# Kernel tuning notes

Hardware: AMD Instinct MI355X
Metric: run time of the kernel (lower is better)

## Reference

```python
import jax, jax.numpy as jnp
import numpy as np

B, S, D = 8, 2048, 512
UNITS = 512

def setup_inputs() -> dict:
    key = jax.random.key(0)
    k1, k2, k3, k4 = jax.random.split(key, 4)
    x = jax.random.normal(k1, (B, S, D), dtype=jnp.float32)
    # glorot-like scale for weights
    scale = 1.0 / np.sqrt(D)
    W_q = jax.random.normal(k2, (D, UNITS), dtype=jnp.float32) * scale
    W_k = jax.random.normal(k3, (D, UNITS), dtype=jnp.float32) * scale
    W_v = jax.random.normal(k4, (D, UNITS), dtype=jnp.float32) * scale
    return {"x": x, "W_q": W_q, "W_k": W_k, "W_v": W_v}

def reference(x, W_q, W_k, W_v):
    # Q,K,V: [B,S,U]
    Q = jnp.einsum('bsd,du->bsu', x, W_q)
    Km = jnp.einsum('bsd,du->bsu', x, W_k)
    V = jnp.einsum('bsd,du->bsu', x, W_v)
    units = W_q.shape[-1]
    # scores: [B,S,S] = Q @ K^T / sqrt(units)
    scores = jnp.einsum('bqu,bku->bqk', Q, Km) / jnp.sqrt(jnp.float32(units))
    attn = jax.nn.softmax(scores, axis=-1)
    # output: [B,S,U]
    return jnp.einsum('bqk,bku->bqu', attn, V)
```

## Files before the change

kernel.cpp:

```cpp
#include <hip/hip_runtime.h>
#include <math.h>

#define BN 8
#define SN 2048
#define DN 512
#define UN 512
#define MN (BN*SN)

typedef _Float16 f16;
typedef _Float16 f16x8 __attribute__((ext_vector_type(8)));
typedef _Float16 f16x4 __attribute__((ext_vector_type(4)));
typedef _Float16 f16x2 __attribute__((ext_vector_type(2)));
typedef float    f32x4 __attribute__((ext_vector_type(4)));

#define SCALE 0.044194173824159216f
#define LOG2E 1.4426950408889634f
#define DEFER_THR 8.0f

#define CVT_PK(a, b) __builtin_bit_cast(f16x2, __builtin_amdgcn_cvt_pkrtz((a), (b)))

#define BAR_LGKM() do {                                         \
  asm volatile("s_waitcnt lgkmcnt(0)" ::: "memory");            \
  __builtin_amdgcn_s_barrier();                                 \
  __builtin_amdgcn_sched_barrier(0);                            \
} while (0)

__device__ __forceinline__ void gload_lds16(const f16* g, f16* l) {
  __builtin_amdgcn_global_load_lds(
      (const __attribute__((address_space(1))) unsigned int*)g,
      (__attribute__((address_space(3))) unsigned int*)l, 16, 0, 0);
}

__global__ __launch_bounds__(256) void cvt_w_kernel(const float* __restrict__ Wq,
                                                    const float* __restrict__ Wk,
                                                    const float* __restrict__ Wv,
                                                    f16* __restrict__ Wt) {
  const float* W = blockIdx.y == 0 ? Wq : (blockIdx.y == 1 ? Wk : Wv);
  const float s = blockIdx.y == 0 ? SCALE : 1.0f;
  f16* o = Wt + (size_t)blockIdx.y * DN * UN;
  int t = blockIdx.x * 256 + threadIdx.x;
  int r  = t >> 7;
  int c4 = (t & 127) * 4;
  float4 v = *(const float4*)(W + (size_t)r * UN + c4);
  o[(size_t)(c4 + 0) * DN + r] = (f16)(v.x * s);
  o[(size_t)(c4 + 1) * DN + r] = (f16)(v.y * s);
  o[(size_t)(c4 + 2) * DN + r] = (f16)(v.z * s);
  o[(size_t)(c4 + 3) * DN + r] = (f16)(v.w * s);
}

__global__ __launch_bounds__(256) void qkv_gemm(const float* __restrict__ x,
                                                const f16* __restrict__ Wt,
                                                f16* __restrict__ Qh,
                                                f16* __restrict__ Kh,
                                                f16* __restrict__ Vt) {
  __shared__ __align__(16) f16 As[128 * 32];
  __shared__ __align__(16) f16 Bs[128 * 32];

  const int tid = threadIdx.x;
  const int w = tid >> 6, lane = tid & 63;
  const int l15 = lane & 15, lh = lane >> 4;
  const int m0 = blockIdx.x * 128;
  const int n0 = blockIdx.y * 128;
  const int widx = blockIdx.z;
  const f16* Wbase = Wt + (size_t)widx * DN * UN;

  const int wr = (w >> 1) * 64, wc = (w & 1) * 64;
  f32x4 acc[4][4] = {};

  const int ra = tid >> 1, ha = tid & 1;
  const int akey = (ra >> 1) & 3;
  const int s0 = (ha * 2) ^ akey, s1 = (ha * 2 + 1) ^ akey;
  const float* xrow = x + (size_t)(m0 + ra) * DN + ha * 16;

  for (int kk = 0; kk < 16; ++kk) {
    const int k0 = kk * 32;

#pragma unroll
    for (int q = 0; q < 2; ++q) {
      int j = q * 256 + tid;
      int r = j >> 2, cs = j & 3;
      int c = cs ^ ((r >> 1) & 3);
      f16* bbase = &Bs[(q * 256 + w * 64) * 8];
      gload_lds16(Wbase + (size_t)(n0 + r) * DN + k0 + c * 8, bbase);
    }

    {
      const float* xs = xrow + k0;
      float4 f0 = *(const float4*)(xs + 0);
      float4 f1 = *(const float4*)(xs + 4);
      float4 f2 = *(const float4*)(xs + 8);
      float4 f3 = *(const float4*)(xs + 12);
      f16x8 lo = { (f16)f0.x, (f16)f0.y, (f16)f0.z, (f16)f0.w,
                   (f16)f1.x, (f16)f1.y, (f16)f1.z, (f16)f1.w };
      f16x8 hi = { (f16)f2.x, (f16)f2.y, (f16)f2.z, (f16)f2.w,
                   (f16)f3.x, (f16)f3.y, (f16)f3.z, (f16)f3.w };
      *(f16x8*)&As[ra * 32 + s0 * 8] = lo;
      *(f16x8*)&As[ra * 32 + s1 * 8] = hi;
    }
    __syncthreads();

    f16x8 a[4], bfr[4];
#pragma unroll
    for (int m = 0; m < 4; ++m) {
      int row = wr + m * 16 + l15;
      int ch = lh ^ ((row >> 1) & 3);
      a[m] = *(const f16x8*)&As[row * 32 + ch * 8];
    }
#pragma unroll
    for (int n = 0; n < 4; ++n) {
      int row = wc + n * 16 + l15;
      int ch = lh ^ ((row >> 1) & 3);
      bfr[n] = *(const f16x8*)&Bs[row * 32 + ch * 8];
    }
#pragma unroll
    for (int m = 0; m < 4; ++m)
#pragma unroll
      for (int n = 0; n < 4; ++n)
        acc[m][n] = __builtin_amdgcn_mfma_f32_16x16x32_f16(a[m], bfr[n], acc[m][n], 0, 0, 0);
    __syncthreads();
  }

  if (widx == 2) {
#pragma unroll
    for (int m = 0; m < 4; ++m) {
      int g = m0 + wr + m * 16 + lh * 4;
      int bb = g >> 11;
      int ss = g & 2047;
#pragma unroll
      for (int n = 0; n < 4; ++n) {
        int u = n0 + wc + n * 16 + l15;
        f16x4 pv = { (f16)acc[m][n][0], (f16)acc[m][n][1],
                     (f16)acc[m][n][2], (f16)acc[m][n][3] };
        *(f16x4*)(Vt + ((size_t)bb * UN + u) * SN + ss) = pv;
      }
    }
  } else {
    f16* O = (widx == 0) ? Qh : Kh;
#pragma unroll
    for (int m = 0; m < 4; ++m)
#pragma unroll
      for (int n = 0; n < 4; ++n)
#pragma unroll
        for (int j = 0; j < 4; ++j)
          O[(size_t)(m0 + wr + m * 16 + lh * 4 + j) * UN + (n0 + wc + n * 16 + l15)] =
              (f16)acc[m][n][j];
  }
}

__global__ __launch_bounds__(512, 2) void attn_kernel(const f16* __restrict__ Qh,
                                                      const f16* __restrict__ Kh,
                                                      const f16* __restrict__ Vt,
                                                      float* __restrict__ out) {
  __shared__ __align__(16) f16 Ks[2][64 * 512];
  __shared__ __align__(16) f16 Ps[2][64 * 72];
  __shared__ float redm[2][4][16];
  __shared__ float redl[2][4][16];

  const int tid = threadIdx.x;
  const int w = tid >> 6, lane = tid & 63;
  const int l15 = lane & 15, lh = lane >> 4;
  const int bid = blockIdx.x;
  const int b = bid & 7;
  const int q0 = (bid >> 3) * 64;
  const int rb = w >> 1;
  const int cs = w & 1;

  const f16* Kbat = Kh + (size_t)b * SN * DN;
  const f16* Vbat = Vt + (size_t)b * UN * SN;

  const f16* Qbase = Qh + (size_t)(b * SN + q0 + rb * 16 + l15) * DN;
  f16x8 qf[16];
#pragma unroll
  for (int kc = 0; kc < 16; ++kc)
    qf[kc] = *(const f16x8*)(Qbase + kc * 32 + lh * 8);

  f32x4 acc[4][4] = {};
  float mj[4] = { -1e30f, -1e30f, -1e30f, -1e30f };
  float rsA[4] = { 1.f, 1.f, 1.f, 1.f };
  bool pend = false;
  float mrow = -1e30f, lrow = 0.f;

  const f16* vbase = Vbat + (size_t)(w * 64 + l15) * SN + lh * 8;
  f16x8 vreg[4][2];

#pragma unroll
  for (int q = 0; q < 8; ++q) {
    int r = w * 8 + q;
    gload_lds16(Kbat + (size_t)r * DN + (lane ^ (r & 7)) * 8, &Ks[0][r * 512]);
  }
  asm volatile("s_waitcnt vmcnt(0)" ::: "memory");
  __builtin_amdgcn_s_barrier();
  __builtin_amdgcn_sched_barrier(0);

  const int kswz = l15 & 7;

  for (int t = 0; t < 32; ++t) {
    const int cur = t & 1;
    const int kv0 = t * 64;

    if (t < 31) {
#pragma unroll
      for (int q = 0; q < 8; ++q) {
        int r = w * 8 + q;
        gload_lds16(Kbat + (size_t)(kv0 + 64 + r) * DN + (lane ^ (r & 7)) * 8,
                    &Ks[cur ^ 1][r * 512]);
      }
    }

    f32x4 sc0 = {}, sc1 = {};
    const int r0 = cs * 32 + l15;
    __builtin_amdgcn_s_setprio(1);
#pragma unroll
    for (int kc = 0; kc < 16; ++kc) {
      int ch = ((kc * 4 + lh) ^ kswz) * 8;
      f16x8 k0 = *(const f16x8*)&Ks[cur][r0 * 512 + ch];
      f16x8 k1 = *(const f16x8*)&Ks[cur][(r0 + 16) * 512 + ch];
      sc0 = __builtin_amdgcn_mfma_f32_16x16x32_f16(k0, qf[kc], sc0, 0, 0, 0);
      sc1 = __builtin_amdgcn_mfma_f32_16x16x32_f16(k1, qf[kc], sc1, 0, 0, 0);
    }
    __builtin_amdgcn_s_setprio(0);

    float pm = fmaxf(fmaxf(fmaxf(sc0[0], sc0[1]), fmaxf(sc0[2], sc0[3])),
                     fmaxf(fmaxf(sc1[0], sc1[1]), fmaxf(sc1[2], sc1[3])));
    pm = fmaxf(pm, __shfl_xor(pm, 16, 64));
    pm = fmaxf(pm, __shfl_xor(pm, 32, 64));
    if (lh == 0) redm[cs][rb][l15] = pm;
    BAR_LGKM();

    if (t > 0) {
      if (pend) {
#pragma unroll
        for (int qt = 0; qt < 4; ++qt)
#pragma unroll
          for (int ut = 0; ut < 4; ++ut) {
            acc[ut][qt][0] *= rsA[qt]; acc[ut][qt][1] *= rsA[qt];
            acc[ut][qt][2] *= rsA[qt]; acc[ut][qt][3] *= rsA[qt];
          }
        pend = false;
      }
      __builtin_amdgcn_s_setprio(1);
#pragma unroll
      for (int ks = 0; ks < 2; ++ks) {
#pragma unroll
        for (int qt = 0; qt < 4; ++qt) {
          f16x8 pf = *(const f16x8*)&Ps[cur ^ 1][(qt * 16 + l15) * 72 + ks * 32 + lh * 8];
#pragma unroll
          for (int ut = 0; ut < 4; ++ut)
            acc[ut][qt] = __builtin_amdgcn_mfma_f32_16x16x32_f16(vreg[ut][ks], pf,
                                                                 acc[ut][qt], 0, 0, 0);
        }
      }
      __builtin_amdgcn_s_setprio(0);
    }

#pragma unroll
    for (int ut = 0; ut < 4; ++ut)
#pragma unroll
      for (int ks = 0; ks < 2; ++ks)
        vreg[ut][ks] = *(const f16x8*)(vbase + (size_t)(ut * 16) * SN + kv0 + ks * 32);

    float mn[4];
    bool need = false;
#pragma unroll
    for (int qt = 0; qt < 4; ++qt) {
      mn[qt] = fmaxf(mj[qt], fmaxf(redm[0][qt][l15], redm[1][qt][l15]));
      need = need || (mn[qt] > mj[qt] + DEFER_THR);
    }
    if (__any(need)) {
#pragma unroll
      for (int qt = 0; qt < 4; ++qt) {
        rsA[qt] = exp2f((mj[qt] - mn[qt]) * LOG2E);
        mj[qt] = mn[qt];
      }
      pend = true;
      float rsr = exp2f((mrow - mj[rb]) * LOG2E);
      mrow = mj[rb];
      lrow *= rsr;
    }

    float p[8];
#pragma unroll
    for (int j = 0; j < 4; ++j) {
      p[j]     = exp2f((sc0[j] - mrow) * LOG2E);
      p[4 + j] = exp2f((sc1[j] - mrow) * LOG2E);
    }
    float ts = (p[0] + p[1]) + (p[2] + p[3]) + (p[4] + p[5]) + (p[6] + p[7]);
    ts += __shfl_xor(ts, 16, 64);
    ts += __shfl_xor(ts, 32, 64);
    lrow += ts;

    const int pbase = (rb * 16 + l15) * 72 + cs * 32 + lh * 4;
    *(f16x2*)&Ps[cur][pbase +  0] = CVT_PK(p[0], p[1]);
    *(f16x2*)&Ps[cur][pbase +  2] = CVT_PK(p[2], p[3]);
    *(f16x2*)&Ps[cur][pbase + 16] = CVT_PK(p[4], p[5]);
    *(f16x2*)&Ps[cur][pbase + 18] = CVT_PK(p[6], p[7]);

    asm volatile("s_waitcnt vmcnt(8) lgkmcnt(0)" ::: "memory");
    __builtin_amdgcn_s_barrier();
    __builtin_amdgcn_sched_barrier(0);
  }

  if (pend) {
#pragma unroll
    for (int qt = 0; qt < 4; ++qt)
#pragma unroll
      for (int ut = 0; ut < 4; ++ut) {
        acc[ut][qt][0] *= rsA[qt]; acc[ut][qt][1] *= rsA[qt];
        acc[ut][qt][2] *= rsA[qt]; acc[ut][qt][3] *= rsA[qt];
      }
  }
#pragma unroll
  for (int ks = 0; ks < 2; ++ks) {
#pragma unroll
    for (int qt = 0; qt < 4; ++qt) {
      f16x8 pf = *(const f16x8*)&Ps[1][(qt * 16 + l15) * 72 + ks * 32 + lh * 8];
#pragma unroll
      for (int ut = 0; ut < 4; ++ut)
        acc[ut][qt] = __builtin_amdgcn_mfma_f32_16x16x32_f16(vreg[ut][ks], pf,
                                                             acc[ut][qt], 0, 0, 0);
    }
  }

  if (lh == 0) redl[cs][rb][l15] = lrow;
  __syncthreads();
#pragma unroll
  for (int qt = 0; qt < 4; ++qt) {
    float linv = 1.0f / (redl[0][qt][l15] + redl[1][qt][l15]);
    float* orow = out + (size_t)(b * SN + q0 + qt * 16 + l15) * UN + w * 64 + lh * 4;
#pragma unroll
    for (int ut = 0; ut < 4; ++ut) {
      f32x4 o = acc[ut][qt];
      o[0] *= linv; o[1] *= linv; o[2] *= linv; o[3] *= linv;
      *(f32x4*)(orow + ut * 16) = o;
    }
  }
}

extern "C" void kernel_launch(void* const* d_in, const int* in_sizes, int n_in,
                              void* d_out, int out_size, void* d_ws, size_t ws_size,
                              hipStream_t stream) {
  const float* x  = (const float*)d_in[0];
  const float* Wq = (const float*)d_in[1];
  const float* Wk = (const float*)d_in[2];
  const float* Wv = (const float*)d_in[3];
  float* out = (float*)d_out;

  f16* Wt  = (f16*)d_ws;
  f16* Qh  = Wt + (size_t)3 * DN * UN;
  f16* Kh  = Qh + (size_t)MN * UN;
  f16* Vt  = Kh + (size_t)MN * UN;

  cvt_w_kernel<<<dim3(256, 3), 256, 0, stream>>>(Wq, Wk, Wv, Wt);
  qkv_gemm<<<dim3(128, 4, 3), 256, 0, stream>>>(x, Wt, Qh, Kh, Vt);
  attn_kernel<<<256, 512, 0, stream>>>(Qh, Kh, Vt, out);
}
```

Before: 195.4 us.

## Warp-specialize attention into QK/softmax and PV/load wave groups

The attention block is split into 16 waves: 8 waves compute QK^T scores and softmax, and 8 waves issue the K prefetch, load V and run the PV MFMAs. The two groups sync through LDS barriers, so score computation for one tile overlaps the PV accumulation of the previous tile. Register pressure per wave drops because each wave holds only Q fragments or only V/accumulators. The cost is 1024-thread blocks, more barrier traffic, and a possible loss of occupancy if the launch bound of 4 blocks cannot be met given the LDS size.

After: 528.3 us. +170.4%, slower.

```diff
diff --git a/kernel.cpp b/kernel.cpp
--- a/kernel.cpp
+++ b/kernel.cpp
@@ -18,12 +18,6 @@
 #define DEFER_THR 8.0f
 
 #define CVT_PK(a, b) __builtin_bit_cast(f16x2, __builtin_amdgcn_cvt_pkrtz((a), (b)))
-
-#define BAR_LGKM() do {                                         \
-  asm volatile("s_waitcnt lgkmcnt(0)" ::: "memory");            \
-  __builtin_amdgcn_s_barrier();                                 \
-  __builtin_amdgcn_sched_barrier(0);                            \
-} while (0)
 
 __device__ __forceinline__ void gload_lds16(const f16* g, f16* l) {
   __builtin_amdgcn_global_load_lds(
@@ -74,7 +68,6 @@
 
   for (int kk = 0; kk < 16; ++kk) {
     const int k0 = kk * 32;
-
 #pragma unroll
     for (int q = 0; q < 2; ++q) {
       int j = q * 256 + tid;
@@ -83,7 +76,6 @@
       f16* bbase = &Bs[(q * 256 + w * 64) * 8];
       gload_lds16(Wbase + (size_t)(n0 + r) * DN + k0 + c * 8, bbase);
     }
-
     {
       const float* xs = xrow + k0;
       float4 f0 = *(const float4*)(xs + 0);
@@ -147,10 +139,10 @@
   }
 }
 
-__global__ __launch_bounds__(512, 2) void attn_kernel(const f16* __restrict__ Qh,
-                                                      const f16* __restrict__ Kh,
-                                                      const f16* __restrict__ Vt,
-                                                      float* __restrict__ out) {
+__global__ __launch_bounds__(1024, 4) void attn_kernel(const f16* __restrict__ Qh,
+                                                       const f16* __restrict__ Kh,
+                                                       const f16* __restrict__ Vt,
+                                                       float* __restrict__ out) {
   __shared__ __align__(16) f16 Ks[2][64 * 512];
   __shared__ __align__(16) f16 Ps[2][64 * 72];
   __shared__ float redm[2][4][16];
@@ -162,102 +154,117 @@
   const int bid = blockIdx.x;
   const int b = bid & 7;
   const int q0 = (bid >> 3) * 64;
-  const int rb = w >> 1;
+  const bool qk = (w < 8);
+  const int rb = (w >> 1) & 3;
   const int cs = w & 1;
+  const int wp = w & 7;
 
   const f16* Kbat = Kh + (size_t)b * SN * DN;
   const f16* Vbat = Vt + (size_t)b * UN * SN;
 
-  const f16* Qbase = Qh + (size_t)(b * SN + q0 + rb * 16 + l15) * DN;
+#pragma unroll
+  for (int q = 0; q < 4; ++q) {
+    int r = w * 4 + q;
+    gload_lds16(Kbat + (size_t)r * DN + (lane ^ (r & 7)) * 8, &Ks[0][r * 512]);
+  }
+
   f16x8 qf[16];
-#pragma unroll
-  for (int kc = 0; kc < 16; ++kc)
-    qf[kc] = *(const f16x8*)(Qbase + kc * 32 + lh * 8);
-
+  f16x8 vreg[4][2];
   f32x4 acc[4][4] = {};
   float mj[4] = { -1e30f, -1e30f, -1e30f, -1e30f };
   float rsA[4] = { 1.f, 1.f, 1.f, 1.f };
   bool pend = false;
   float mrow = -1e30f, lrow = 0.f;
 
-  const f16* vbase = Vbat + (size_t)(w * 64 + l15) * SN + lh * 8;
-  f16x8 vreg[4][2];
-
-#pragma unroll
-  for (int q = 0; q < 8; ++q) {
-    int r = w * 8 + q;
-    gload_lds16(Kbat + (size_t)r * DN + (lane ^ (r & 7)) * 8, &Ks[0][r * 512]);
-  }
-  asm volatile("s_waitcnt vmcnt(0)" ::: "memory");
+  const f16* vbase = Vbat + (size_t)(wp * 64 + l15) * SN + lh * 8;
+
+  if (qk) {
+    const f16* Qbase = Qh + (size_t)(b * SN + q0 + rb * 16 + l15) * DN;
+#pragma unroll
+    for (int kc = 0; kc < 16; ++kc)
+      qf[kc] = *(const f16x8*)(Qbase + kc * 32 + lh * 8);
+    asm volatile("s_waitcnt vmcnt(16)" ::: "memory");
+  } else {
+#pragma unroll
+    for (int ut = 0; ut < 4; ++ut)
+#pragma unroll
+      for (int ks = 0; ks < 2; ++ks)
+        vreg[ut][ks] = *(const f16x8*)(vbase + (size_t)(ut * 16) * SN + ks * 32);
+    asm volatile("s_waitcnt vmcnt(8)" ::: "memory");
+  }
   __builtin_amdgcn_s_barrier();
   __builtin_amdgcn_sched_barrier(0);
 
   const int kswz = l15 & 7;
+  f32x4 sc0, sc1;
 
   for (int t = 0; t < 32; ++t) {
     const int cur = t & 1;
     const int kv0 = t * 64;
 
-    if (t < 31) {
-#pragma unroll
-      for (int q = 0; q < 8; ++q) {
-        int r = w * 8 + q;
-        gload_lds16(Kbat + (size_t)(kv0 + 64 + r) * DN + (lane ^ (r & 7)) * 8,
-                    &Ks[cur ^ 1][r * 512]);
-      }
-    }
-
-    f32x4 sc0 = {}, sc1 = {};
-    const int r0 = cs * 32 + l15;
-    __builtin_amdgcn_s_setprio(1);
-#pragma unroll
-    for (int kc = 0; kc < 16; ++kc) {
-      int ch = ((kc * 4 + lh) ^ kswz) * 8;
-      f16x8 k0 = *(const f16x8*)&Ks[cur][r0 * 512 + ch];
-      f16x8 k1 = *(const f16x8*)&Ks[cur][(r0 + 16) * 512 + ch];
-      sc0 = __builtin_amdgcn_mfma_f32_16x16x32_f16(k0, qf[kc], sc0, 0, 0, 0);
-      sc1 = __builtin_amdgcn_mfma_f32_16x16x32_f16(k1, qf[kc], sc1, 0, 0, 0);
-    }
-    __builtin_amdgcn_s_setprio(0);
-
-    float pm = fmaxf(fmaxf(fmaxf(sc0[0], sc0[1]), fmaxf(sc0[2], sc0[3])),
-                     fmaxf(fmaxf(sc1[0], sc1[1]), fmaxf(sc1[2], sc1[3])));
-    pm = fmaxf(pm, __shfl_xor(pm, 16, 64));
-    pm = fmaxf(pm, __shfl_xor(pm, 32, 64));
-    if (lh == 0) redm[cs][rb][l15] = pm;
-    BAR_LGKM();
-
-    if (t > 0) {
-      if (pend) {
-#pragma unroll
-        for (int qt = 0; qt < 4; ++qt)
-#pragma unroll
-          for (int ut = 0; ut < 4; ++ut) {
-            acc[ut][qt][0] *= rsA[qt]; acc[ut][qt][1] *= rsA[qt];
-            acc[ut][qt][2] *= rsA[qt]; acc[ut][qt][3] *= rsA[qt];
+    if (qk) {
+      sc0 = (f32x4){};
+      sc1 = (f32x4){};
+      const int r0 = cs * 32 + l15;
+      __builtin_amdgcn_s_setprio(1);
+#pragma unroll
+      for (int kc = 0; kc < 16; ++kc) {
+        int ch = ((kc * 4 + lh) ^ kswz) * 8;
+        f16x8 k0 = *(const f16x8*)&Ks[cur][r0 * 512 + ch];
+        f16x8 k1 = *(const f16x8*)&Ks[cur][(r0 + 16) * 512 + ch];
+        sc0 = __builtin_amdgcn_mfma_f32_16x16x32_f16(k0, qf[kc], sc0, 0, 0, 0);
+        sc1 = __builtin_amdgcn_mfma_f32_16x16x32_f16(k1, qf[kc], sc1, 0, 0, 0);
+      }
+      __builtin_amdgcn_s_setprio(0);
+      float pm = fmaxf(fmaxf(fmaxf(sc0[0], sc0[1]), fmaxf(sc0[2], sc0[3])),
+                       fmaxf(fmaxf(sc1[0], sc1[1]), fmaxf(sc1[2], sc1[3])));
+      pm = fmaxf(pm, __shfl_xor(pm, 16, 64));
+      pm = fmaxf(pm, __shfl_xor(pm, 32, 64));
+      if (lh == 0) redm[cs][rb][l15] = pm;
+    } else {
+      if (t < 31) {
+#pragma unroll
+        for (int q = 0; q < 8; ++q) {
+          int r = wp * 8 + q;
+          gload_lds16(Kbat + (size_t)(kv0 + 64 + r) * DN + (lane ^ (r & 7)) * 8,
+                      &Ks[cur ^ 1][r * 512]);
+        }
+      }
+      if (t > 0) {
+        if (pend) {
+#pragma unroll
+          for (int qt = 0; qt < 4; ++qt)
+#pragma unroll
+            for (int ut = 0; ut < 4; ++ut) {
+              acc[ut][qt][0] *= rsA[qt]; acc[ut][qt][1] *= rsA[qt];
+              acc[ut][qt][2] *= rsA[qt]; acc[ut][qt][3] *= rsA[qt];
+            }
+          pend = false;
+        }
+        __builtin_amdgcn_s_setprio(1);
+#pragma unroll
+        for (int ks = 0; ks < 2; ++ks) {
+#pragma unroll
+          for (int qt = 0; qt < 4; ++qt) {
+            f16x8 pf = *(const f16x8*)&Ps[cur ^ 1][(qt * 16 + l15) * 72 + ks * 32 + lh * 8];
+#pragma unroll
+            for (int ut = 0; ut < 4; ++ut)
+              acc[ut][qt] = __builtin_amdgcn_mfma_f32_16x16x32_f16(vreg[ut][ks], pf,
+                                                                   acc[ut][qt], 0, 0, 0);
           }
-        pend = false;
-      }
-      __builtin_amdgcn_s_setprio(1);
-#pragma unroll
-      for (int ks = 0; ks < 2; ++ks) {
-#pragma unroll
-        for (int qt = 0; qt < 4; ++qt) {
-          f16x8 pf = *(const f16x8*)&Ps[cur ^ 1][(qt * 16 + l15) * 72 + ks * 32 + lh * 8];
-#pragma unroll
-          for (int ut = 0; ut < 4; ++ut)
-            acc[ut][qt] = __builtin_amdgcn_mfma_f32_16x16x32_f16(vreg[ut][ks], pf,
-                                                                 acc[ut][qt], 0, 0, 0);
-        }
-      }
-      __builtin_amdgcn_s_setprio(0);
-    }
-
-#pragma unroll
-    for (int ut = 0; ut < 4; ++ut)
-#pragma unroll
-      for (int ks = 0; ks < 2; ++ks)
-        vreg[ut][ks] = *(const f16x8*)(vbase + (size_t)(ut * 16) * SN + kv0 + ks * 32);
+        }
+        __builtin_amdgcn_s_setprio(0);
+      }
+#pragma unroll
+      for (int ut = 0; ut < 4; ++ut)
+#pragma unroll
+        for (int ks = 0; ks < 2; ++ks)
+          vreg[ut][ks] = *(const f16x8*)(vbase + (size_t)(ut * 16) * SN + kv0 + ks * 32);
+    }
+
+    asm volatile("s_waitcnt lgkmcnt(0)" ::: "memory");
+    __builtin_amdgcn_s_barrier();
+    __builtin_amdgcn_sched_barrier(0);
 
     float mn[4];
     bool need = false;
@@ -266,72 +273,82 @@
       mn[qt] = fmaxf(mj[qt], fmaxf(redm[0][qt][l15], redm[1][qt][l15]));
       need = need || (mn[qt] > mj[qt] + DEFER_THR);
     }
-    if (__any(need)) {
-#pragma unroll
-      for (int qt = 0; qt < 4; ++qt) {
-        rsA[qt] = exp2f((mj[qt] - mn[qt]) * LOG2E);
-        mj[qt] = mn[qt];
-      }
-      pend = true;
-      float rsr = exp2f((mrow - mj[rb]) * LOG2E);
-      mrow = mj[rb];
-      lrow *= rsr;
-    }
-
-    float p[8];
-#pragma unroll
-    for (int j = 0; j < 4; ++j) {
-      p[j]     = exp2f((sc0[j] - mrow) * LOG2E);
-      p[4 + j] = exp2f((sc1[j] - mrow) * LOG2E);
-    }
-    float ts = (p[0] + p[1]) + (p[2] + p[3]) + (p[4] + p[5]) + (p[6] + p[7]);
-    ts += __shfl_xor(ts, 16, 64);
-    ts += __shfl_xor(ts, 32, 64);
-    lrow += ts;
-
-    const int pbase = (rb * 16 + l15) * 72 + cs * 32 + lh * 4;
-    *(f16x2*)&Ps[cur][pbase +  0] = CVT_PK(p[0], p[1]);
-    *(f16x2*)&Ps[cur][pbase +  2] = CVT_PK(p[2], p[3]);
-    *(f16x2*)&Ps[cur][pbase + 16] = CVT_PK(p[4], p[5]);
-    *(f16x2*)&Ps[cur][pbase + 18] = CVT_PK(p[6], p[7]);
-
-    asm volatile("s_waitcnt vmcnt(8) lgkmcnt(0)" ::: "memory");
+    if (qk) {
+      if (__any(need)) {
+#pragma unroll
+        for (int qt = 0; qt < 4; ++qt) mj[qt] = mn[qt];
+        float rsr = exp2f((mrow - mj[rb]) * LOG2E);
+        mrow = mj[rb];
+        lrow *= rsr;
+      }
+      float p[8];
+#pragma unroll
+      for (int j = 0; j < 4; ++j) {
+        p[j]     = exp2f((sc0[j] - mrow) * LOG2E);
+        p[4 + j] = exp2f((sc1[j] - mrow) * LOG2E);
+      }
+      float ts = (p[0] + p[1]) + (p[2] + p[3]) + (p[4] + p[5]) + (p[6] + p[7]);
+      ts += __shfl_xor(ts, 16, 64);
+      ts += __shfl_xor(ts, 32, 64);
+      lrow += ts;
+      const int pbase = (rb * 16 + l15) * 72 + cs * 32 + lh * 4;
+      *(f16x2*)&Ps[cur][pbase +  0] = CVT_PK(p[0], p[1]);
+      *(f16x2*)&Ps[cur][pbase +  2] = CVT_PK(p[2], p[3]);
+      *(f16x2*)&Ps[cur][pbase + 16] = CVT_PK(p[4], p[5]);
+      *(f16x2*)&Ps[cur][pbase + 18] = CVT_PK(p[6], p[7]);
+      asm volatile("s_waitcnt lgkmcnt(0)" ::: "memory");
+    } else {
+      if (__any(need)) {
+#pragma unroll
+        for (int qt = 0; qt < 4; ++qt) {
+          rsA[qt] = exp2f((mj[qt] - mn[qt]) * LOG2E);
+          mj[qt] = mn[qt];
+        }
+        pend = true;
+      }
+      asm volatile("s_waitcnt vmcnt(8) lgkmcnt(0)" ::: "memory");
+    }
     __builtin_amdgcn_s_barrier();
     __builtin_amdgcn_sched_barrier(0);
   }
 
-  if (pend) {
-#pragma unroll
-    for (int qt = 0; qt < 4; ++qt)
+  if (qk) {
+    if (lh == 0) redl[cs][rb][l15] = lrow;
+  } else {
+    if (pend) {
+#pragma unroll
+      for (int qt = 0; qt < 4; ++qt)
+#pragma unroll
+        for (int ut = 0; ut < 4; ++ut) {
+          acc[ut][qt][0] *= rsA[qt]; acc[ut][qt][1] *= rsA[qt];
+          acc[ut][qt][2] *= rsA[qt]; acc[ut][qt][3] *= rsA[qt];
+        }
+    }
+#pragma unroll
+    for (int ks = 0; ks < 2; ++ks) {
+#pragma unroll
+      for (int qt = 0; qt < 4; ++qt) {
+        f16x8 pf = *(const f16x8*)&Ps[1][(qt * 16 + l15) * 72 + ks * 32 + lh * 8];
+#pragma unroll
+        for (int ut = 0; ut < 4; ++ut)
+          acc[ut][qt] = __builtin_amdgcn_mfma_f32_16x16x32_f16(vreg[ut][ks], pf,
+                                                               acc[ut][qt], 0, 0, 0);
+      }
+    }
+  }
+  __syncthreads();
+
+  if (!qk) {
+#pragma unroll
+    for (int qt = 0; qt < 4; ++qt) {
+      float linv = 1.0f / (redl[0][qt][l15] + redl[1][qt][l15]);
+      float* orow = out + (size_t)(b * SN + q0 + qt * 16 + l15) * UN + wp * 64 + lh * 4;
 #pragma unroll
       for (int ut = 0; ut < 4; ++ut) {
-        acc[ut][qt][0] *= rsA[qt]; acc[ut][qt][1] *= rsA[qt];
-        acc[ut][qt][2] *= rsA[qt]; acc[ut][qt][3] *= rsA[qt];
-      }
-  }
-#pragma unroll
-  for (int ks = 0; ks < 2; ++ks) {
-#pragma unroll
-    for (int qt = 0; qt < 4; ++qt) {
-      f16x8 pf = *(const f16x8*)&Ps[1][(qt * 16 + l15) * 72 + ks * 32 + lh * 8];
-#pragma unroll
-      for (int ut = 0; ut < 4; ++ut)
-        acc[ut][qt] = __builtin_amdgcn_mfma_f32_16x16x32_f16(vreg[ut][ks], pf,
-                                                             acc[ut][qt], 0, 0, 0);
-    }
-  }
-
-  if (lh == 0) redl[cs][rb][l15] = lrow;
-  __syncthreads();
-#pragma unroll
-  for (int qt = 0; qt < 4; ++qt) {
-    float linv = 1.0f / (redl[0][qt][l15] + redl[1][qt][l15]);
-    float* orow = out + (size_t)(b * SN + q0 + qt * 16 + l15) * UN + w * 64 + lh * 4;
-#pragma unroll
-    for (int ut = 0; ut < 4; ++ut) {
-      f32x4 o = acc[ut][qt];
-      o[0] *= linv; o[1] *= linv; o[2] *= linv; o[3] *= linv;
-      *(f32x4*)(orow + ut * 16) = o;
+        f32x4 o = acc[ut][qt];
+        o[0] *= linv; o[1] *= linv; o[2] *= linv; o[3] *= linv;
+        *(f32x4*)(orow + ut * 16) = o;
+      }
     }
   }
 }
@@ -352,5 +369,5 @@
 
   cvt_w_kernel<<<dim3(256, 3), 256, 0, stream>>>(Wq, Wk, Wv, Wt);
   qkv_gemm<<<dim3(128, 4, 3), 256, 0, stream>>>(x, Wt, Qh, Kh, Vt);
-  attn_kernel<<<256, 512, 0, stream>>>(Qh, Kh, Vt, out);
-}
+  attn_kernel<<<256, 1024, 0, stream>>>(Qh, Kh, Vt, out);
+}
```
